# Kernel optimization log

Measured on AMD Instinct MI355X. Metric: run time of the kernel, lower is better.

## Reference

```python
import jax, jax.numpy as jnp
import numpy as np

G = 8    # deformable groups
K2 = 9   # 3x3 kernel taps


def conv3(x, w, b=None):
    # 3x3, stride 1, SAME padding, NCHW
    y = jax.lax.conv_general_dilated(x, w, (1, 1), 'SAME',
                                     dimension_numbers=('NCHW', 'OIHW', 'NCHW'))
    if b is not None:
        y = y + b[None, :, None, None]
    return y


def deform_conv(x, offset, wgt):
    # DCNv1: x [B,C,H,W], offset [B, G*K2*2, H, W] (per tap: dy,dx), wgt [O,C,3,3]
    B, C, H, W = x.shape
    Cpg = C // G
    off = offset.reshape(B, G, K2, 2, H, W)
    dy, dx = off[:, :, :, 0], off[:, :, :, 1]                      # [B,G,K2,H,W]
    ky = jnp.repeat(jnp.arange(-1, 2), 3).astype(x.dtype)          # tap row offsets
    kx = jnp.tile(jnp.arange(-1, 2), 3).astype(x.dtype)            # tap col offsets
    py = dy + jnp.arange(H, dtype=x.dtype)[None, None, None, :, None] + ky[None, None, :, None, None]
    px = dx + jnp.arange(W, dtype=x.dtype)[None, None, None, None, :] + kx[None, None, :, None, None]
    xg = x.reshape(B, G, Cpg, H * W)
    y0 = jnp.floor(py)
    x0 = jnp.floor(px)

    def corner(yc, xc):
        m = ((yc >= 0) & (yc <= H - 1) & (xc >= 0) & (xc <= W - 1)).astype(x.dtype)
        yi = jnp.clip(yc, 0, H - 1).astype(jnp.int32)
        xi = jnp.clip(xc, 0, W - 1).astype(jnp.int32)
        idx = (yi * W + xi).reshape(B, G, -1)                      # [B,G,K2*H*W]
        v = jax.vmap(jax.vmap(lambda f, i: f[:, i]))(xg, idx)      # [B,G,Cpg,K2*H*W]
        return v.reshape(B, G, Cpg, K2, H, W), m

    v00, m00 = corner(y0, x0)
    v01, m01 = corner(y0, x0 + 1)
    v10, m10 = corner(y0 + 1, x0)
    v11, m11 = corner(y0 + 1, x0 + 1)
    wy = py - y0
    wx = px - x0
    w00 = ((1 - wy) * (1 - wx) * m00)[:, :, None]   # [B,G,1,K2,H,W]
    w01 = ((1 - wy) * wx * m01)[:, :, None]
    w10 = (wy * (1 - wx) * m10)[:, :, None]
    w11 = (wy * wx * m11)[:, :, None]
    sampled = v00 * w00 + v01 * w01 + v10 * w10 + v11 * w11        # [B,G,Cpg,K2,H,W]
    O = wgt.shape[0]
    return jnp.einsum('bgckhw,ogck->bohw', sampled, wgt.reshape(O, G, Cpg, K2))


def setup_inputs() -> dict:
    key = jax.random.key(0)
    ks = jax.random.split(key, 16)

    def he(k, shape):
        # torch init: normal(0, sqrt(2 / (kh*kw*out_ch)))
        o = shape[-4]
        return jax.random.normal(k, shape, jnp.float32) * np.float32(np.sqrt(2.0 / (9 * o)))

    inp = {
        'x': jax.random.normal(ks[0], (2, 5, 3, 128, 128), jnp.float32),
        'conv_first_w': he(ks[1], (64, 3, 3, 3)),
        'conv_first_b': jax.random.normal(ks[2], (64,), jnp.float32) * 0.01,
        'res_w1': he(ks[3], (5, 64, 64, 3, 3)),
        'res_b1': jax.random.normal(ks[4], (5, 64), jnp.float32) * 0.01,
        'res_w2': he(ks[5], (5, 64, 64, 3, 3)),
        'res_b2': jax.random.normal(ks[6], (5, 64), jnp.float32) * 0.01,
        'cr_w': he(ks[7], (64, 128, 3, 3)),
        'cr_b': jax.random.normal(ks[8], (64,), jnp.float32) * 0.01,
        'off_w': he(ks[9], (4, 144, 64, 3, 3)),
        'off_b': jax.random.normal(ks[10], (4, 144), jnp.float32) * 0.01,
        'dconv_w': he(ks[11], (4, 64, 64, 3, 3)),
        'recon_w': he(ks[12], (3, 64, 3, 3)),
        'recon_b': jax.random.normal(ks[13], (3,), jnp.float32) * 0.01,
    }
    return inp


def reference(x, conv_first_w, conv_first_b, res_w1, res_b1, res_w2, res_b2,
              cr_w, cr_b, off_w, off_b, dconv_w, recon_w, recon_b):
    B, N, C, H, W = x.shape
    center = N // 2
    # shared feature trunk over all frames
    out = jax.nn.relu(conv3(x.reshape(B * N, C, H, W), conv_first_w, conv_first_b))
    for i in range(res_w1.shape[0]):
        r = jax.nn.relu(conv3(out, res_w1[i], res_b1[i]))
        out = out + conv3(r, res_w2[i], res_b2[i])
    out = out.reshape(B, N, 64, H, W)
    ref = out[:, center]                                   # [B,64,H,W]
    supp_idx = np.array([i for i in range(N) if i != center])
    supp = out[:, supp_idx].reshape(B * (N - 1), 64, H, W)
    ref_rep = jnp.broadcast_to(ref[:, None], (B, N - 1, 64, H, W)).reshape(B * (N - 1), 64, H, W)
    # alignment cascade (vectorized over the N-1 support frames)
    fea = conv3(jnp.concatenate([ref_rep, supp], axis=1), cr_w, cr_b)
    fea = deform_conv(fea, conv3(fea, off_w[0], off_b[0]), dconv_w[0])
    fea = deform_conv(fea, conv3(fea, off_w[1], off_b[1]), dconv_w[1])
    fea = deform_conv(supp, conv3(fea, off_w[2], off_b[2]), dconv_w[2])
    aligned = deform_conv(fea, conv3(fea, off_w[3], off_b[3]), dconv_w[3])
    im = conv3(aligned, recon_w, recon_b)                  # [B*(N-1),3,H,W]
    ims = im.reshape(B, N - 1, 3, H, W)
    feas = fea.reshape(B, N - 1, 64, H, W)
    x_center = x[:, center]
    lrs = jnp.concatenate([ims[:, :center], x_center[:, None], ims[:, center:]], axis=1)
    feats = jnp.concatenate([feas[:, :center], ref[:, None], feas[:, center:]], axis=1)
    return lrs, feats
```

## Files before the change

kernel.cpp:

```cpp
#include <hip/hip_runtime.h>

#define HH 128
#define WW 128
#define HWX (HH*WW)

using f32x4 = __attribute__((ext_vector_type(4))) float;
using f16x8 = __attribute__((ext_vector_type(8))) _Float16;

__device__ __forceinline__ unsigned short f16bits(_Float16 h) {
  union { _Float16 f; unsigned short u; } v; v.f = h; return v.u;
}

__device__ __forceinline__ int swz(int pos, int q) {
  return pos * 32 + (((q + pos + (pos >> 2)) & 3) << 3);
}

__global__ __launch_bounds__(256) void wprep_k(
    const float* __restrict__ src, unsigned short* __restrict__ dhi,
    unsigned short* __restrict__ dlo, int O, int I, int L)
{
  int idx = blockIdx.x * 256 + threadIdx.x;
  int tot = L * O * I * 9;
  if (idx >= tot) return;
  int per = O * I * 9;
  int layer = idx / per;
  int r = idx - layer * per;
  int o = r / (I * 9);
  int r2 = r - o * (I * 9);
  int i = r2 / 9, k = r2 - i * 9;
  float v = src[idx];
  _Float16 h = (_Float16)v;
  _Float16 l = (_Float16)(v - (float)h);
  long di = (long)layer * per + ((long)k * O + o) * I + i;
  dhi[di] = f16bits(h);
  dlo[di] = f16bits(l);
}

__global__ __launch_bounds__(256) void dwprep_k(
    const float* __restrict__ src, unsigned short* __restrict__ dhi,
    unsigned short* __restrict__ dlo)
{
  int idx = blockIdx.x * 256 + threadIdx.x;
  if (idx >= 147456) return;
  int l = idx / 36864;
  int rem = idx - l * 36864;
  int o = rem / 576;
  int rem2 = rem - o * 576;
  int r = rem2 / 9, k2 = rem2 - r * 9;
  float v = src[idx];
  _Float16 h = (_Float16)v;
  _Float16 lo = (_Float16)(v - (float)h);
  long di = (((long)l * 9 + k2) * 64 + o) * 64 + r;
  dhi[di] = f16bits(h);
  dlo[di] = f16bits(lo);
}

template<int CBLK, int NFRAG, bool RELU, bool ADD, bool CRMODE>
__global__ __launch_bounds__(256, 2) void conv_mfma_k(
    const float* __restrict__ in, const unsigned short* __restrict__ whi,
    const unsigned short* __restrict__ wlo,
    const float* __restrict__ bias, const float* __restrict__ res,
    float* __restrict__ out, int Cout, int nslice, int img_in0, int img_out0)
{
  constexpr int CIN = CBLK * 32;
  constexpr int OCB = NFRAG * 16;
  constexpr int SLAB = OCB * 32;
  __shared__ __align__(16) unsigned short s_in[2 * 10880];
  __shared__ __align__(16) unsigned short s_w[2][2 * SLAB];

  const int tid = threadIdx.x;
  const int lane = tid & 63;
  const int wv = tid >> 6;
  const int m16 = lane & 15, q = lane >> 4;
  const int iz = blockIdx.z / nslice, slice = blockIdx.z % nslice;
  const int oc_blk0 = slice * OCB;
  const int x0 = blockIdx.x * 32, y0 = blockIdx.y * 8;

  f32x4 acc[4][NFRAG];
#pragma unroll
  for (int mt = 0; mt < 4; ++mt)
#pragma unroll
    for (int nt = 0; nt < NFRAG; ++nt)
#pragma unroll
      for (int i = 0; i < 4; ++i) acc[mt][nt][i] = 0.f;

  int bb = 0, nn = 0;
  const float* inb = in;
  if (CRMODE) {
    int j = img_in0 + iz;
    bb = j >> 2;
    int ns = j & 3;
    nn = ns < 2 ? ns : ns + 1;
  } else {
    inb = in + (long)(img_in0 + iz) * CIN * HWX;
  }

  for (int cb = 0; cb < CBLK; ++cb) {
    const int c0 = cb * 32;
    for (int t = tid; t < 1360; t += 256) {
      int qq = t / 340, pos = t - qq * 340;
      int iy = pos / 34, ix = pos - iy * 34;
      int gy = y0 + iy - 1, gx = x0 + ix - 1;
      bool inr = (gy >= 0 && gy < HH && gx >= 0 && gx < WW);
      const float* src;
      if (CRMODE) {
        int ch = c0 + qq * 8;
        int simg = (ch < 64) ? (bb * 5 + 2) : (bb * 5 + nn);
        src = in + ((long)simg * 64 + (ch & 63)) * HWX + gy * WW + gx;
      } else {
        src = inb + (long)(c0 + qq * 8) * HWX + gy * WW + gx;
      }
      unsigned hi4[4], lo4[4];
#pragma unroll
      for (int j2 = 0; j2 < 4; ++j2) {
        unsigned short hs[2], ls[2];
#pragma unroll
        for (int j = 0; j < 2; ++j) {
          float v = inr ? src[(long)(j2 * 2 + j) * HWX] : 0.f;
          _Float16 h = (_Float16)v;
          _Float16 l = (_Float16)(v - (float)h);
          hs[j] = f16bits(h); ls[j] = f16bits(l);
        }
        hi4[j2] = (unsigned)hs[0] | ((unsigned)hs[1] << 16);
        lo4[j2] = (unsigned)ls[0] | ((unsigned)ls[1] << 16);
      }
      *(uint4*)(s_in + swz(pos, qq)) = make_uint4(hi4[0], hi4[1], hi4[2], hi4[3]);
      *(uint4*)(s_in + 10880 + swz(pos, qq)) =
          make_uint4(lo4[0], lo4[1], lo4[2], lo4[3]);
    }
    for (int t = tid; t < OCB * 4; t += 256) {
      int qq = t & 3, ocl = t >> 2;
      long so = ((long)0 * Cout + oc_blk0 + ocl) * CIN + c0 + qq * 8;
      *(uint4*)(s_w[0] + swz(ocl, qq)) = *(const uint4*)(whi + so);
      *(uint4*)(s_w[0] + SLAB + swz(ocl, qq)) = *(const uint4*)(wlo + so);
    }
    __syncthreads();

#pragma unroll
    for (int kp = 0; kp < 9; ++kp) {
      if (kp < 8) {
        const int buf = (kp + 1) & 1;
        for (int t = tid; t < OCB * 4; t += 256) {
          int qq = t & 3, ocl = t >> 2;
          long so = ((long)(kp + 1) * Cout + oc_blk0 + ocl) * CIN + c0 + qq * 8;
          *(uint4*)(s_w[buf] + swz(ocl, qq)) = *(const uint4*)(whi + so);
          *(uint4*)(s_w[buf] + SLAB + swz(ocl, qq)) = *(const uint4*)(wlo + so);
        }
      }
      const unsigned short* wb = s_w[kp & 1];
      const int dy = kp / 3, dx = kp - dy * 3;
      f16x8 bhi[NFRAG], blo[NFRAG];
#pragma unroll
      for (int nt = 0; nt < NFRAG; ++nt) {
        int pw = nt * 16 + m16;
        bhi[nt] = *(const f16x8*)(wb + swz(pw, q));
        blo[nt] = *(const f16x8*)(wb + SLAB + swz(pw, q));
      }
#pragma unroll
      for (int mt = 0; mt < 4; ++mt) {
        int r = 2 * wv + (mt >> 1), h = mt & 1;
        int pos = (r + dy) * 34 + h * 16 + m16 + dx;
        f16x8 ahi = *(const f16x8*)(s_in + swz(pos, q));
        f16x8 alo = *(const f16x8*)(s_in + 10880 + swz(pos, q));
#pragma unroll
        for (int nt = 0; nt < NFRAG; ++nt) {
          acc[mt][nt] = __builtin_amdgcn_mfma_f32_16x16x32_f16(
              ahi, blo[nt], acc[mt][nt], 0, 0, 0);
          acc[mt][nt] = __builtin_amdgcn_mfma_f32_16x16x32_f16(
              alo, bhi[nt], acc[mt][nt], 0, 0, 0);
          acc[mt][nt] = __builtin_amdgcn_mfma_f32_16x16x32_f16(
              ahi, bhi[nt], acc[mt][nt], 0, 0, 0);
        }
      }
      __syncthreads();
    }
  }

  const int img_o = img_out0 + iz;
#pragma unroll
  for (int mt = 0; mt < 4; ++mt) {
    int r = 2 * wv + (mt >> 1), h = mt & 1;
    int y = y0 + r;
    int xb = x0 + h * 16 + q * 4;
#pragma unroll
    for (int nt = 0; nt < NFRAG; ++nt) {
      int oc = oc_blk0 + nt * 16 + m16;
      if (oc < Cout) {
        float bsv = bias[oc];
        long base = ((long)img_o * Cout + oc) * HWX + (long)y * WW + xb;
#pragma unroll
        for (int i = 0; i < 4; ++i) {
          float v = acc[mt][nt][i] + bsv;
          if (RELU) v = fmaxf(v, 0.f);
          if (ADD) v += res[base + i];
          out[base + i] = v;
        }
      }
    }
  }
}

template<int CIN, int CK, int OCB, bool RELU, bool ADD>
__global__ __launch_bounds__(256) void conv3x3_k(
    const float* __restrict__ in, const float* __restrict__ wgt,
    const float* __restrict__ bias, const float* __restrict__ res,
    float* __restrict__ out, int Cout, int nslice, int img_in0, int img_out0)
{
  __shared__ __align__(16) float s_in[CK][34][34];
  __shared__ __align__(16) float s_w[CK * 9 * OCB];

  const int tid = threadIdx.x;
  const int tx = tid & 31;
  const int ty = tid >> 5;
  const int iz = blockIdx.z / nslice;
  const int slice = blockIdx.z % nslice;
  const int oc0 = slice * OCB;
  const int x0 = blockIdx.x * 32;
  const int y0 = blockIdx.y * 32;

  float acc[4][OCB];
#pragma unroll
  for (int r = 0; r < 4; ++r)
#pragma unroll
    for (int o = 0; o < OCB; ++o) acc[r][o] = 0.f;

  const float* inb = in + (long)(img_in0 + iz) * CIN * HWX;

  for (int c0 = 0; c0 < CIN; c0 += CK) {
    __syncthreads();
    for (int idx = tid; idx < CK * 34 * 34; idx += 256) {
      int c = idx / 1156;
      int rem = idx % 1156;
      int iy = rem / 34, ix = rem % 34;
      int gy = y0 + iy - 1, gx = x0 + ix - 1;
      float v = 0.f;
      if (gy >= 0 && gy < HH && gx >= 0 && gx < WW)
        v = inb[(long)(c0 + c) * HWX + gy * WW + gx];
      s_in[c][iy][ix] = v;
    }
    for (int idx = tid; idx < CK * 9 * OCB; idx += 256) {
      int oc = idx % OCB;
      int ck = idx / OCB;
      int c = ck / 9, k = ck % 9;
      int ocg = oc0 + oc;
      float v = 0.f;
      if (ocg < Cout) v = wgt[((long)ocg * CIN + c0 + c) * 9 + k];
      s_w[idx] = v;
    }
    __syncthreads();

    for (int c = 0; c < CK; ++c) {
#pragma unroll
      for (int k = 0; k < 9; ++k) {
        const int ky = k / 3, kx = k % 3;
        float v0 = s_in[c][ty + ky][tx + kx];
        float v1 = s_in[c][ty + 8 + ky][tx + kx];
        float v2 = s_in[c][ty + 16 + ky][tx + kx];
        float v3 = s_in[c][ty + 24 + ky][tx + kx];
        const float4* wp = (const float4*)&s_w[(c * 9 + k) * OCB];
#pragma unroll
        for (int o4 = 0; o4 < OCB / 4; ++o4) {
          float4 w4 = wp[o4];
          acc[0][o4 * 4 + 0] += v0 * w4.x; acc[0][o4 * 4 + 1] += v0 * w4.y;
          acc[0][o4 * 4 + 2] += v0 * w4.z; acc[0][o4 * 4 + 3] += v0 * w4.w;
          acc[1][o4 * 4 + 0] += v1 * w4.x; acc[1][o4 * 4 + 1] += v1 * w4.y;
          acc[1][o4 * 4 + 2] += v1 * w4.z; acc[1][o4 * 4 + 3] += v1 * w4.w;
          acc[2][o4 * 4 + 0] += v2 * w4.x; acc[2][o4 * 4 + 1] += v2 * w4.y;
          acc[2][o4 * 4 + 2] += v2 * w4.z; acc[2][o4 * 4 + 3] += v2 * w4.w;
          acc[3][o4 * 4 + 0] += v3 * w4.x; acc[3][o4 * 4 + 1] += v3 * w4.y;
          acc[3][o4 * 4 + 2] += v3 * w4.z; acc[3][o4 * 4 + 3] += v3 * w4.w;
        }
      }
    }
  }

#pragma unroll
  for (int o = 0; o < OCB; ++o) {
    int ocg = oc0 + o;
    if (ocg < Cout) {
      float b = bias ? bias[ocg] : 0.f;
      long base = ((long)(img_out0 + iz) * Cout + ocg) * HWX;
#pragma unroll
      for (int r = 0; r < 4; ++r) {
        int y = y0 + ty + 8 * r;
        float v = acc[r][o] + b;
        if (RELU) v = fmaxf(v, 0.f);
        long ia = base + (long)y * WW + x0 + tx;
        if (ADD) v += res[ia];
        out[ia] = v;
      }
    }
  }
}

__global__ __launch_bounds__(256) void regroup_k(
    const float* __restrict__ src, float* __restrict__ dst, int supp_mode)
{
  int idx = blockIdx.x * 256 + threadIdx.x;
  int c = idx & 7;
  int p = (idx >> 3) & 16383;
  int g = (idx >> 17) & 7;
  int img = idx >> 20;
  int simg = img;
  if (supp_mode) {
    int b = img >> 2, ns = img & 3;
    simg = b * 5 + (ns < 2 ? ns : ns + 1);
  }
  dst[idx] = src[((simg * 64 + g * 8 + c) * HWX) + p];
}

__device__ __forceinline__ void bilin8(const float* __restrict__ sg,
                                       float py, float px, float* sv)
{
  float y0f = floorf(py), x0f = floorf(px);
  float wy = py - y0f, wx = px - x0f;
  float y1f = y0f + 1.f, x1f = x0f + 1.f;
  float my0 = (y0f >= 0.f && y0f <= 127.f) ? 1.f : 0.f;
  float my1 = (y1f >= 0.f && y1f <= 127.f) ? 1.f : 0.f;
  float mx0 = (x0f >= 0.f && x0f <= 127.f) ? 1.f : 0.f;
  float mx1 = (x1f >= 0.f && x1f <= 127.f) ? 1.f : 0.f;
  int yi0 = (int)fminf(fmaxf(y0f, 0.f), 127.f);
  int yi1 = (int)fminf(fmaxf(y1f, 0.f), 127.f);
  int xi0 = (int)fminf(fmaxf(x0f, 0.f), 127.f);
  int xi1 = (int)fminf(fmaxf(x1f, 0.f), 127.f);
  float w00 = (1.f - wy) * (1.f - wx) * my0 * mx0;
  float w01 = (1.f - wy) * wx * my0 * mx1;
  float w10 = wy * (1.f - wx) * my1 * mx0;
  float w11 = wy * wx * my1 * mx1;
  const float4* p00 = (const float4*)(sg + ((long)yi0 * WW + xi0) * 8);
  const float4* p01 = (const float4*)(sg + ((long)yi0 * WW + xi1) * 8);
  const float4* p10 = (const float4*)(sg + ((long)yi1 * WW + xi0) * 8);
  const float4* p11 = (const float4*)(sg + ((long)yi1 * WW + xi1) * 8);
  float4 a00 = p00[0], b00 = p00[1];
  float4 a01 = p01[0], b01 = p01[1];
  float4 a10 = p10[0], b10 = p10[1];
  float4 a11 = p11[0], b11 = p11[1];
  sv[0] = w00 * a00.x + w01 * a01.x + w10 * a10.x + w11 * a11.x;
  sv[1] = w00 * a00.y + w01 * a01.y + w10 * a10.y + w11 * a11.y;
  sv[2] = w00 * a00.z + w01 * a01.z + w10 * a10.z + w11 * a11.z;
  sv[3] = w00 * a00.w + w01 * a01.w + w10 * a10.w + w11 * a11.w;
  sv[4] = w00 * b00.x + w01 * b01.x + w10 * b10.x + w11 * b11.x;
  sv[5] = w00 * b00.y + w01 * b01.y + w10 * b10.y + w11 * b11.y;
  sv[6] = w00 * b00.z + w01 * b01.z + w10 * b10.z + w11 * b11.z;
  sv[7] = w00 * b00.w + w01 * b01.w + w10 * b10.w + w11 * b11.w;
}

__global__ __launch_bounds__(256) void deform_mfma_k(
    const float* __restrict__ srcg, const float* __restrict__ off,
    const unsigned short* __restrict__ wh, const unsigned short* __restrict__ wl,
    float* __restrict__ out, int img0, int cmask, int cshift)
{
  __shared__ __align__(16) float s_off[9216];
  __shared__ __align__(16) unsigned short s_bh[4096];
  __shared__ __align__(16) unsigned short s_bl[4096];
  const int tid = threadIdx.x;
  const int lane = tid & 63;
  const int wv = tid >> 6;
  const int m16 = lane & 15, q = lane >> 4;
  const int bid = blockIdx.x;
  const int iz = bid & cmask;
  const int tile = bid >> cshift;
  const int img = img0 + iz;
  const int tp0 = tile * 64;
  const int pl = wv * 16 + m16;
  const int p = tp0 + pl;
  const float fy = (float)(p >> 7), fx = (float)(p & 127);
  const int rot = 8 * (m16 & 7);

  {
    const float* ob = off + (long)iz * 144 * HWX + tp0;
    for (int t = tid; t < 2304; t += 256) {
      int c = t >> 4, j = t & 15;
      *(float4*)(s_off + c * 64 + 4 * j) =
          *(const float4*)(ob + (long)c * HWX + 4 * j);
    }
  }

  f32x4 acc[4];
#pragma unroll
  for (int nt = 0; nt < 4; ++nt)
#pragma unroll
    for (int i = 0; i < 4; ++i) acc[nt][i] = 0.f;

  for (int k2 = 0; k2 < 9; ++k2) {
    __syncthreads();
    for (int t = tid; t < 512; t += 256) {
      int o = t >> 3, j = t & 7;
      int d = o * 64 + ((8 * j + 8 * (o & 7)) & 63);
      long so = ((long)k2 * 64 + o) * 64 + 8 * j;
      *(uint4*)(s_bh + d) = *(const uint4*)(wh + so);
      *(uint4*)(s_bl + d) = *(const uint4*)(wl + so);
    }
    __syncthreads();
    const float kyf = (float)(k2 / 3 - 1), kxf = (float)(k2 % 3 - 1);
#pragma unroll
    for (int s = 0; s < 2; ++s) {
      const int g = 4 * s + q;
      float dyv = s_off[(g * 18 + 2 * k2) * 64 + pl];
      float dxv = s_off[(g * 18 + 2 * k2 + 1) * 64 + pl];
      float sv[8];
      bilin8(srcg + (long)(img * 8 + g) * HWX * 8,
             dyv + fy + kyf, dxv + fx + kxf, sv);
      f16x8 ah, al;
#pragma unroll
      for (int j = 0; j < 8; ++j) {
        _Float16 h = (_Float16)sv[j];
        _Float16 l = (_Float16)(sv[j] - (float)h);
        ah[j] = h; al[j] = l;
      }
      const int roff = (32 * s + 8 * q + rot) & 63;
#pragma unroll
      for (int nt = 0; nt < 4; ++nt) {
        int o = nt * 16 + m16;
        f16x8 bh = *(const f16x8*)(s_bh + o * 64 + roff);
        f16x8 bl = *(const f16x8*)(s_bl + o * 64 + roff);
        acc[nt] = __builtin_amdgcn_mfma_f32_16x16x32_f16(ah, bl, acc[nt], 0, 0, 0);
        acc[nt] = __builtin_amdgcn_mfma_f32_16x16x32_f16(al, bh, acc[nt], 0, 0, 0);
        acc[nt] = __builtin_amdgcn_mfma_f32_16x16x32_f16(ah, bh, acc[nt], 0, 0, 0);
      }
    }
  }

  const long pb = tp0 + wv * 16 + q * 4;
#pragma unroll
  for (int nt = 0; nt < 4; ++nt) {
    int oc = nt * 16 + m16;
    float4 v;
    v.x = acc[nt][0]; v.y = acc[nt][1]; v.z = acc[nt][2]; v.w = acc[nt][3];
    *(float4*)(out + ((long)img * 64 + oc) * HWX + pb) = v;
  }
}

__global__ __launch_bounds__(256) void assemble_k(
    const float* __restrict__ x, const float* __restrict__ im,
    const float* __restrict__ out0, const float* __restrict__ fea,
    float* __restrict__ out)
{
  int idx = blockIdx.x * 256 + threadIdx.x;
  if (idx < 491520) {
    int within = idx % 49152;
    int n = (idx / 49152) % 5;
    int b = idx / (49152 * 5);
    float v;
    if (n == 2) v = x[(b * 5 + 2) * 49152 + within];
    else {
      int j = b * 4 + (n < 2 ? n : n - 1);
      v = im[j * 49152 + within];
    }
    out[idx] = v;
  } else if (idx < 10977280) {
    int idx2 = idx - 491520;
    int within = idx2 % 1048576;
    int n = (idx2 / 1048576) % 5;
    int b = idx2 / (1048576 * 5);
    float v;
    if (n == 2) v = out0[(b * 5 + 2) * 1048576 + within];
    else {
      int j = b * 4 + (n < 2 ? n : n - 1);
      v = fea[j * 1048576 + within];
    }
    out[idx] = v;
  }
}

extern "C" void kernel_launch(void* const* d_in, const int* in_sizes, int n_in,
                              void* d_out, int out_size, void* d_ws, size_t ws_size,
                              hipStream_t stream) {
  const float* x   = (const float*)d_in[0];
  const float* cfw = (const float*)d_in[1];
  const float* cfb = (const float*)d_in[2];
  const float* rw1 = (const float*)d_in[3];
  const float* rb1 = (const float*)d_in[4];
  const float* rw2 = (const float*)d_in[5];
  const float* rb2 = (const float*)d_in[6];
  const float* crw = (const float*)d_in[7];
  const float* crb = (const float*)d_in[8];
  const float* ofw = (const float*)d_in[9];
  const float* ofb = (const float*)d_in[10];
  const float* dcw = (const float*)d_in[11];
  const float* rcw = (const float*)d_in[12];
  const float* rcb = (const float*)d_in[13];
  float* out = (float*)d_out;

  unsigned short* WH = (unsigned short*)d_ws;
  unsigned short* WL = WH + 774144;
  unsigned short* DH = WH + 1548288;
  unsigned short* DL = DH + 147456;
  const long W_res1 = 0, W_res2 = 184320, W_cr = 368640, W_off = 442368;

  float* A = (float*)d_ws + 921600;
  float* C = A + 10485760;
  float* D = C + 8388608;
  float* F = D + 8388608;
  float* OFF = F + 8388608;
  float* r = C;
  float* im = D;

  const size_t fixedF = 921600UL + 10485760UL + 3UL * 8388608UL;
  int chunk = 8;
  while (chunk > 1 && (fixedF + (size_t)chunk * 2359296UL) * sizeof(float) > ws_size)
    chunk >>= 1;
  int cshift = (chunk == 8) ? 3 : (chunk == 4) ? 2 : (chunk == 2) ? 1 : 0;

  dim3 blk(256);

  wprep_k<<<720, blk, 0, stream>>>(rw1, WH + W_res1, WL + W_res1, 64, 64, 5);
  wprep_k<<<720, blk, 0, stream>>>(rw2, WH + W_res2, WL + W_res2, 64, 64, 5);
  wprep_k<<<288, blk, 0, stream>>>(crw, WH + W_cr, WL + W_cr, 64, 128, 1);
  wprep_k<<<1296, blk, 0, stream>>>(ofw, WH + W_off, WL + W_off, 144, 64, 4);
  dwprep_k<<<576, blk, 0, stream>>>(dcw, DH, DL);

  conv3x3_k<3, 3, 16, true, false><<<dim3(4, 4, 40), blk, 0, stream>>>(
      x, cfw, cfb, nullptr, A, 64, 4, 0, 0);

  for (int i = 0; i < 5; ++i) {
    conv_mfma_k<2, 4, true, false, false><<<dim3(4, 16, 10), blk, 0, stream>>>(
        A, WH + W_res1 + (long)i * 36864, WL + W_res1 + (long)i * 36864,
        rb1 + i * 64, nullptr, r, 64, 1, 0, 0);
    conv_mfma_k<2, 4, false, true, false><<<dim3(4, 16, 10), blk, 0, stream>>>(
        r, WH + W_res2 + (long)i * 36864, WL + W_res2 + (long)i * 36864,
        rb2 + i * 64, A, A, 64, 1, 0, 0);
  }

  conv_mfma_k<4, 4, false, false, true><<<dim3(4, 16, 8), blk, 0, stream>>>(
      A, WH + W_cr, WL + W_cr, crb, nullptr, C, 64, 1, 0, 0);

  auto off_deform = [&](const float* fea_in, const float* grouped,
                        int layer, float* outp) {
    for (int i0 = 0; i0 < 8; i0 += chunk) {
      conv_mfma_k<2, 3, false, false, false>
          <<<dim3(4, 16, chunk * 3), blk, 0, stream>>>(
              fea_in, WH + W_off + (long)layer * 82944,
              WL + W_off + (long)layer * 82944, ofb + layer * 144,
              nullptr, OFF, 144, 3, i0, 0);
      deform_mfma_k<<<dim3(256 * chunk), blk, 0, stream>>>(
          grouped, OFF, DH + (long)layer * 36864, DL + (long)layer * 36864,
          outp, i0, chunk - 1, cshift);
    }
  };

  regroup_k<<<32768, blk, 0, stream>>>(C, D, 0);
  off_deform(C, D, 0, C);

  regroup_k<<<32768, blk, 0, stream>>>(C, D, 0);
  off_deform(C, D, 1, C);

  regroup_k<<<32768, blk, 0, stream>>>(A, D, 1);
  off_deform(C, D, 2, F);

  regroup_k<<<32768, blk, 0, stream>>>(F, D, 0);
  off_deform(F, D, 3, C);

  conv3x3_k<64, 8, 4, false, false><<<dim3(4, 4, 8), blk, 0, stream>>>(
      C, rcw, rcb, nullptr, im, 3, 1, 0, 0);

  assemble_k<<<42880, blk, 0, stream>>>(x, im, A, F, out);
}
```

Baseline: 2.005 ms.

## Software-pipeline deformable gather loads and double-buffer weight staging

Restructures the deformable conv MFMA kernel so the bilinear corner gathers for the next tap-group are issued into registers before the current one is processed, and offsets are prefetched three steps ahead straight from global memory instead of being staged in LDS. Per-tap weights are double-buffered in LDS, which drops one barrier per tap. The aim is to hide gather latency behind MFMA work and shrink LDS use so more blocks fit per CU, at the cost of more live registers (16 float4 corner values plus offsets), which could lower occupancy or cause spills.

```diff
diff --git a/kernel.cpp b/kernel.cpp
--- a/kernel.cpp
+++ b/kernel.cpp
@@ -309,50 +309,12 @@
   dst[idx] = src[((simg * 64 + g * 8 + c) * HWX) + p];
 }
 
-__device__ __forceinline__ void bilin8(const float* __restrict__ sg,
-                                       float py, float px, float* sv)
-{
-  float y0f = floorf(py), x0f = floorf(px);
-  float wy = py - y0f, wx = px - x0f;
-  float y1f = y0f + 1.f, x1f = x0f + 1.f;
-  float my0 = (y0f >= 0.f && y0f <= 127.f) ? 1.f : 0.f;
-  float my1 = (y1f >= 0.f && y1f <= 127.f) ? 1.f : 0.f;
-  float mx0 = (x0f >= 0.f && x0f <= 127.f) ? 1.f : 0.f;
-  float mx1 = (x1f >= 0.f && x1f <= 127.f) ? 1.f : 0.f;
-  int yi0 = (int)fminf(fmaxf(y0f, 0.f), 127.f);
-  int yi1 = (int)fminf(fmaxf(y1f, 0.f), 127.f);
-  int xi0 = (int)fminf(fmaxf(x0f, 0.f), 127.f);
-  int xi1 = (int)fminf(fmaxf(x1f, 0.f), 127.f);
-  float w00 = (1.f - wy) * (1.f - wx) * my0 * mx0;
-  float w01 = (1.f - wy) * wx * my0 * mx1;
-  float w10 = wy * (1.f - wx) * my1 * mx0;
-  float w11 = wy * wx * my1 * mx1;
-  const float4* p00 = (const float4*)(sg + ((long)yi0 * WW + xi0) * 8);
-  const float4* p01 = (const float4*)(sg + ((long)yi0 * WW + xi1) * 8);
-  const float4* p10 = (const float4*)(sg + ((long)yi1 * WW + xi0) * 8);
-  const float4* p11 = (const float4*)(sg + ((long)yi1 * WW + xi1) * 8);
-  float4 a00 = p00[0], b00 = p00[1];
-  float4 a01 = p01[0], b01 = p01[1];
-  float4 a10 = p10[0], b10 = p10[1];
-  float4 a11 = p11[0], b11 = p11[1];
-  sv[0] = w00 * a00.x + w01 * a01.x + w10 * a10.x + w11 * a11.x;
-  sv[1] = w00 * a00.y + w01 * a01.y + w10 * a10.y + w11 * a11.y;
-  sv[2] = w00 * a00.z + w01 * a01.z + w10 * a10.z + w11 * a11.z;
-  sv[3] = w00 * a00.w + w01 * a01.w + w10 * a10.w + w11 * a11.w;
-  sv[4] = w00 * b00.x + w01 * b01.x + w10 * b10.x + w11 * b11.x;
-  sv[5] = w00 * b00.y + w01 * b01.y + w10 * b10.y + w11 * b11.y;
-  sv[6] = w00 * b00.z + w01 * b01.z + w10 * b10.z + w11 * b11.z;
-  sv[7] = w00 * b00.w + w01 * b01.w + w10 * b10.w + w11 * b11.w;
-}
-
 __global__ __launch_bounds__(256) void deform_mfma_k(
     const float* __restrict__ srcg, const float* __restrict__ off,
     const unsigned short* __restrict__ wh, const unsigned short* __restrict__ wl,
     float* __restrict__ out, int img0, int cmask, int cshift)
 {
-  __shared__ __align__(16) float s_off[9216];
-  __shared__ __align__(16) unsigned short s_bh[4096];
-  __shared__ __align__(16) unsigned short s_bl[4096];
+  __shared__ __align__(16) unsigned short s_w[2][2 * 4096];
   const int tid = threadIdx.x;
   const int lane = tid & 63;
   const int wv = tid >> 6;
@@ -362,19 +324,86 @@
   const int tile = bid >> cshift;
   const int img = img0 + iz;
   const int tp0 = tile * 64;
-  const int pl = wv * 16 + m16;
-  const int p = tp0 + pl;
+  const int p = tp0 + wv * 16 + m16;
   const float fy = (float)(p >> 7), fx = (float)(p & 127);
   const int rot = 8 * (m16 & 7);
 
-  {
-    const float* ob = off + (long)iz * 144 * HWX + tp0;
-    for (int t = tid; t < 2304; t += 256) {
-      int c = t >> 4, j = t & 15;
-      *(float4*)(s_off + c * 64 + 4 * j) =
-          *(const float4*)(ob + (long)c * HWX + 4 * j);
-    }
-  }
+  const float* offb = off + (long)iz * 144 * HWX + p;
+  const float* sgq[2];
+  sgq[0] = srcg + (long)(img * 8 + q) * HWX * 8;
+  sgq[1] = srcg + (long)(img * 8 + 4 + q) * HWX * 8;
+
+  float dyr[3], dxr[3];
+  float pyr[2], pxr[2];
+  float4 cr[2][8];
+
+#define LOAD_OFF(T, SLOT) { \
+    const float* ob_ = offb + ((long)(4 * ((T) & 1) + q) * 18 + 2 * ((T) >> 1)) * HWX; \
+    dyr[SLOT] = ob_[0]; dxr[SLOT] = ob_[HWX]; }
+
+#define ISSUE(T, SLOT, OS) { \
+    const int k2_ = (T) >> 1; \
+    float py_ = dyr[OS] + fy + (float)(k2_ / 3 - 1); \
+    float px_ = dxr[OS] + fx + (float)(k2_ % 3 - 1); \
+    pyr[SLOT] = py_; pxr[SLOT] = px_; \
+    float y0f_ = floorf(py_), x0f_ = floorf(px_); \
+    int yi0_ = (int)fminf(fmaxf(y0f_, 0.f), 127.f); \
+    int yi1_ = (int)fminf(fmaxf(y0f_ + 1.f, 0.f), 127.f); \
+    int xi0_ = (int)fminf(fmaxf(x0f_, 0.f), 127.f); \
+    int xi1_ = (int)fminf(fmaxf(x0f_ + 1.f, 0.f), 127.f); \
+    const float* sg_ = sgq[(T) & 1]; \
+    const float4* p00_ = (const float4*)(sg_ + ((long)yi0_ * WW + xi0_) * 8); \
+    const float4* p01_ = (const float4*)(sg_ + ((long)yi0_ * WW + xi1_) * 8); \
+    const float4* p10_ = (const float4*)(sg_ + ((long)yi1_ * WW + xi0_) * 8); \
+    const float4* p11_ = (const float4*)(sg_ + ((long)yi1_ * WW + xi1_) * 8); \
+    cr[SLOT][0] = p00_[0]; cr[SLOT][1] = p00_[1]; \
+    cr[SLOT][2] = p01_[0]; cr[SLOT][3] = p01_[1]; \
+    cr[SLOT][4] = p10_[0]; cr[SLOT][5] = p10_[1]; \
+    cr[SLOT][6] = p11_[0]; cr[SLOT][7] = p11_[1]; }
+
+#define STAGE(K2) { \
+    const int buf_ = (K2) & 1; \
+    for (int t2 = tid; t2 < 512; t2 += 256) { \
+      int o_ = t2 >> 3, j_ = t2 & 7; \
+      int d_ = o_ * 64 + ((8 * j_ + 8 * (o_ & 7)) & 63); \
+      long so_ = ((long)(K2) * 64 + o_) * 64 + 8 * j_; \
+      *(uint4*)(s_w[buf_] + d_) = *(const uint4*)(wh + so_); \
+      *(uint4*)(s_w[buf_] + 4096 + d_) = *(const uint4*)(wl + so_); \
+    } }
+
+#define PROCESS(T, SLOT) { \
+    float py_ = pyr[SLOT], px_ = pxr[SLOT]; \
+    float y0f_ = floorf(py_), x0f_ = floorf(px_); \
+    float wy_ = py_ - y0f_, wx_ = px_ - x0f_; \
+    float my0 = (y0f_ >= 0.f && y0f_ <= 127.f) ? 1.f : 0.f; \
+    float my1 = (y0f_ >= -1.f && y0f_ <= 126.f) ? 1.f : 0.f; \
+    float mx0 = (x0f_ >= 0.f && x0f_ <= 127.f) ? 1.f : 0.f; \
+    float mx1 = (x0f_ >= -1.f && x0f_ <= 126.f) ? 1.f : 0.f; \
+    float w00 = (1.f - wy_) * (1.f - wx_) * my0 * mx0; \
+    float w01 = (1.f - wy_) * wx_ * my0 * mx1; \
+    float w10 = wy_ * (1.f - wx_) * my1 * mx0; \
+    float w11 = wy_ * wx_ * my1 * mx1; \
+    f16x8 ah, al; \
+    _Pragma("unroll") \
+    for (int j = 0; j < 4; ++j) { \
+      float v0 = w00 * ((const float*)&cr[SLOT][0])[j] + w01 * ((const float*)&cr[SLOT][2])[j] \
+               + w10 * ((const float*)&cr[SLOT][4])[j] + w11 * ((const float*)&cr[SLOT][6])[j]; \
+      float v1 = w00 * ((const float*)&cr[SLOT][1])[j] + w01 * ((const float*)&cr[SLOT][3])[j] \
+               + w10 * ((const float*)&cr[SLOT][5])[j] + w11 * ((const float*)&cr[SLOT][7])[j]; \
+      _Float16 h0 = (_Float16)v0; ah[j] = h0; al[j] = (_Float16)(v0 - (float)h0); \
+      _Float16 h1 = (_Float16)v1; ah[4 + j] = h1; al[4 + j] = (_Float16)(v1 - (float)h1); \
+    } \
+    const unsigned short* wb_ = s_w[((T) >> 1) & 1]; \
+    const int roff_ = (32 * ((T) & 1) + 8 * q + rot) & 63; \
+    _Pragma("unroll") \
+    for (int nt = 0; nt < 4; ++nt) { \
+      int o_ = nt * 16 + m16; \
+      f16x8 bh = *(const f16x8*)(wb_ + o_ * 64 + roff_); \
+      f16x8 bl = *(const f16x8*)(wb_ + 4096 + o_ * 64 + roff_); \
+      acc[nt] = __builtin_amdgcn_mfma_f32_16x16x32_f16(ah, bl, acc[nt], 0, 0, 0); \
+      acc[nt] = __builtin_amdgcn_mfma_f32_16x16x32_f16(al, bh, acc[nt], 0, 0, 0); \
+      acc[nt] = __builtin_amdgcn_mfma_f32_16x16x32_f16(ah, bh, acc[nt], 0, 0, 0); \
+    } }
 
   f32x4 acc[4];
 #pragma unroll
@@ -382,44 +411,30 @@
 #pragma unroll
     for (int i = 0; i < 4; ++i) acc[nt][i] = 0.f;
 
+  LOAD_OFF(0, 0);
+  LOAD_OFF(1, 1);
+  ISSUE(0, 0, 0);
+  LOAD_OFF(2, 2);
+  STAGE(0);
+  __syncthreads();
+
+#pragma unroll
   for (int k2 = 0; k2 < 9; ++k2) {
+    if (k2 < 8) STAGE(k2 + 1);
+#pragma unroll
+    for (int s = 0; s < 2; ++s) {
+      const int t = 2 * k2 + s;
+      if (t < 17) ISSUE(t + 1, (t + 1) & 1, (t + 1) % 3);
+      if (t < 15) LOAD_OFF(t + 3, (t + 3) % 3);
+      PROCESS(t, t & 1);
+    }
     __syncthreads();
-    for (int t = tid; t < 512; t += 256) {
-      int o = t >> 3, j = t & 7;
-      int d = o * 64 + ((8 * j + 8 * (o & 7)) & 63);
-      long so = ((long)k2 * 64 + o) * 64 + 8 * j;
-      *(uint4*)(s_bh + d) = *(const uint4*)(wh + so);
-      *(uint4*)(s_bl + d) = *(const uint4*)(wl + so);
-    }
-    __syncthreads();
-    const float kyf = (float)(k2 / 3 - 1), kxf = (float)(k2 % 3 - 1);
-#pragma unroll
-    for (int s = 0; s < 2; ++s) {
-      const int g = 4 * s + q;
-      float dyv = s_off[(g * 18 + 2 * k2) * 64 + pl];
-      float dxv = s_off[(g * 18 + 2 * k2 + 1) * 64 + pl];
-      float sv[8];
-      bilin8(srcg + (long)(img * 8 + g) * HWX * 8,
-             dyv + fy + kyf, dxv + fx + kxf, sv);
-      f16x8 ah, al;
-#pragma unroll
-      for (int j = 0; j < 8; ++j) {
-        _Float16 h = (_Float16)sv[j];
-        _Float16 l = (_Float16)(sv[j] - (float)h);
-        ah[j] = h; al[j] = l;
-      }
-      const int roff = (32 * s + 8 * q + rot) & 63;
-#pragma unroll
-      for (int nt = 0; nt < 4; ++nt) {
-        int o = nt * 16 + m16;
-        f16x8 bh = *(const f16x8*)(s_bh + o * 64 + roff);
-        f16x8 bl = *(const f16x8*)(s_bl + o * 64 + roff);
-        acc[nt] = __builtin_amdgcn_mfma_f32_16x16x32_f16(ah, bl, acc[nt], 0, 0, 0);
-        acc[nt] = __builtin_amdgcn_mfma_f32_16x16x32_f16(al, bh, acc[nt], 0, 0, 0);
-        acc[nt] = __builtin_amdgcn_mfma_f32_16x16x32_f16(ah, bh, acc[nt], 0, 0, 0);
-      }
-    }
-  }
+  }
+
+#undef LOAD_OFF
+#undef ISSUE
+#undef STAGE
+#undef PROCESS
 
   const long pb = tp0 + wv * 16 + q * 4;
 #pragma unroll
```

Result: faster. 1.962 ms (-2.2%).
